# Performance work log

Hardware: AMD Instinct MI355X
Metric: run time of the kernel (lower is better)

Reference implementation:

```python
import jax, jax.numpy as jnp
import numpy as np

def setup_inputs() -> dict:
    key = jax.random.key(0)
    QKV = jax.random.normal(key, (3, 2, 8, 4096, 64), dtype=jnp.float32)
    return {"QKV": QKV}

def reference(QKV):
    Q, K, V = QKV[0], QKV[1], QKV[2]            # each [B, H, N, d]
    scores = jnp.einsum('bhnd,bhmd->bhnm', Q, K)  # full N x N score matrix (no scaling, matching source)
    attn = jax.nn.softmax(scores, axis=-1)
    return jnp.einsum('bhnm,bhmd->bhnd', attn, V)
```

## Files before the change

### kernel.cpp

```cpp
#include <hip/hip_runtime.h>


typedef _Float16 f16x8 __attribute__((ext_vector_type(8)));
typedef _Float16 f16x2 __attribute__((ext_vector_type(2)));
typedef short s16x8 __attribute__((ext_vector_type(8)));
typedef short s16x4 __attribute__((ext_vector_type(4)));
typedef float f32x4 __attribute__((ext_vector_type(4)));

#define NHEADS 16
#define SEQ 4096
#define HDIM 64
#define BR 256
#define NH 4
#define BC 64
#define KP 72
#define PP 72
#define NSPLIT 2
#define MPAD 4.0f

__device__ __forceinline__ float fast_exp2(float x) {
#if __has_builtin(__builtin_amdgcn_exp2f)
  return __builtin_amdgcn_exp2f(x);
#else
  return exp2f(x);
#endif
}

__device__ __forceinline__ f16x2 pkrtz(float a, float b) {
  return __builtin_bit_cast(f16x2, __builtin_amdgcn_cvt_pkrtz(a, b));
}

__device__ __forceinline__ unsigned short f2bf(float f) {
  unsigned u = __builtin_bit_cast(unsigned, f);
  u += 0x7fffu + ((u >> 16) & 1u);
  return (unsigned short)(u >> 16);
}

__device__ __forceinline__ unsigned bfpack2(float a, float b) {
  return (__builtin_bit_cast(unsigned, b) & 0xffff0000u) |
         (__builtin_bit_cast(unsigned, a) >> 16);
}

__global__ __launch_bounds__(256) void prep(const float* __restrict__ QKV,
                                            _Float16* __restrict__ K16,
                                            short* __restrict__ Vt) {
  const size_t tensElems = (size_t)NHEADS * SEQ * HDIM;
  __shared__ __align__(16) short T[64 * KP];
  if (blockIdx.x < 2048) {
    const float* Kf = QKV + tensElems;
    size_t i = ((size_t)blockIdx.x * 256 + threadIdx.x) * 8;
    float4 a = *(const float4*)(Kf + i);
    float4 b = *(const float4*)(Kf + i + 4);
    union { f16x8 v; f16x2 h2[4]; } u;
    u.h2[0] = pkrtz(a.x, a.y);
    u.h2[1] = pkrtz(a.z, a.w);
    u.h2[2] = pkrtz(b.x, b.y);
    u.h2[3] = pkrtz(b.z, b.w);
    *(f16x8*)(K16 + i) = u.v;
  } else {
    const int vb = blockIdx.x - 2048;
    const int bh = vb >> 6;
    const int nt = vb & 63;
    const float* Vh = QKV + 2 * tensElems + (size_t)bh * SEQ * HDIM +
                      (size_t)nt * 64 * HDIM;
    const int t = threadIdx.x;
    #pragma unroll
    for (int p = 0; p < 4; ++p) {
      int idx = t + p * 256;
      int row = idx >> 4, c4 = (idx & 15) << 2;
      float4 v = *(const float4*)(Vh + row * HDIM + c4);
      s16x4 h;
      h[0] = (short)f2bf(v.x); h[1] = (short)f2bf(v.y);
      h[2] = (short)f2bf(v.z); h[3] = (short)f2bf(v.w);
      *(s16x4*)&T[row * KP + c4] = h;
    }
    __syncthreads();
    const int d = t & 63, w = t >> 6;
    s16x8 o0, o1;
    #pragma unroll
    for (int j = 0; j < 8; ++j) o0[j] = T[(w * 16 + j) * KP + d];
    #pragma unroll
    for (int j = 0; j < 8; ++j) o1[j] = T[(w * 16 + 8 + j) * KP + d];
    short* out = Vt + (size_t)bh * HDIM * SEQ + (size_t)d * SEQ + nt * 64 + w * 16;
    *(s16x8*)out = o0;
    *(s16x8*)(out + 8) = o1;
  }
}

__global__ __launch_bounds__(256) void combine2(const _Float16* __restrict__ Op,
                                                const float2* __restrict__ Ml,
                                                float* __restrict__ O) {
  const size_t tensElems = (size_t)NHEADS * SEQ * HDIM;
  size_t t = (size_t)blockIdx.x * 256 + threadIdx.x;
  size_t row = t >> 3;
  int seg = (int)(t & 7) << 3;
  float2 s0 = Ml[row];
  float2 s1 = Ml[(size_t)NHEADS * SEQ + row];
  float Ms = fmaxf(s0.x, s1.x);
  float a0 = fast_exp2(s0.x - Ms) * s0.y;
  float a1 = fast_exp2(s1.x - Ms) * s1.y;
  float inv = 1.0f / (a0 + a1);
  a0 *= inv;
  a1 *= inv;
  f16x8 o0 = *(const f16x8*)(Op + row * HDIM + seg);
  f16x8 o1 = *(const f16x8*)(Op + tensElems + row * HDIM + seg);
  float4 r0, r1;
  r0.x = (float)o0[0] * a0 + (float)o1[0] * a1;
  r0.y = (float)o0[1] * a0 + (float)o1[1] * a1;
  r0.z = (float)o0[2] * a0 + (float)o1[2] * a1;
  r0.w = (float)o0[3] * a0 + (float)o1[3] * a1;
  r1.x = (float)o0[4] * a0 + (float)o1[4] * a1;
  r1.y = (float)o0[5] * a0 + (float)o1[5] * a1;
  r1.z = (float)o0[6] * a0 + (float)o1[6] * a1;
  r1.w = (float)o0[7] * a0 + (float)o1[7] * a1;
  *(float4*)(O + row * HDIM + seg) = r0;
  *(float4*)(O + row * HDIM + seg + 4) = r1;
}

template <bool PRE, bool SPLIT>
__global__ __launch_bounds__(256, 2) void flash_attn(const float* __restrict__ QKV,
                                                     const _Float16* __restrict__ K16g,
                                                     const short* __restrict__ Vt16,
                                                     float* __restrict__ Out,
                                                     _Float16* __restrict__ Opart,
                                                     float2* __restrict__ Ml) {
  const size_t headElems = (size_t)SEQ * HDIM;
  const size_t tensElems = (size_t)NHEADS * headElems;
  const int bh = blockIdx.x & 15;
  const int qt = blockIdx.x >> 4;
  const int split = SPLIT ? blockIdx.y : 0;
  const int ktBeg = SPLIT ? split * (SEQ / BC / NSPLIT) : 0;
  const int ktN = SPLIT ? (SEQ / BC / NSPLIT) : (SEQ / BC);

  const float* Q = QKV + (size_t)bh * headElems;
  const float* Kf = QKV + tensElems + (size_t)bh * headElems;
  const float* Vf = QKV + 2 * tensElems + (size_t)bh * headElems;
  const _Float16* Kg16 = K16g + (size_t)bh * headElems;
  const short* Vg16 = Vt16 + (size_t)bh * headElems;
  float* O = Out + (size_t)bh * headElems;

  const int tid = threadIdx.x;
  const int wave = tid >> 6;
  const int lane = tid & 63;
  const int g = lane >> 4;
  const int l16 = lane & 15;

  __shared__ __align__(16) _Float16 Ks[BC * KP];
  __shared__ __align__(16) short Vs[HDIM * KP];
  __shared__ __align__(16) short Ps[4][NH][16 * PP];

  const float LOG2E = 1.4426950408889634f;
  const int qbase = qt * BR + wave * (16 * NH);
  f16x8 qf[NH][2];
  #pragma unroll
  for (int h = 0; h < NH; ++h) {
    const float* qp = Q + (size_t)(qbase + h * 16 + l16) * HDIM + g * 8;
    #pragma unroll
    for (int c = 0; c < 2; ++c) {
      float4 a = *(const float4*)(qp + c * 32);
      float4 b = *(const float4*)(qp + c * 32 + 4);
      union { f16x8 v; f16x2 h2[4]; } u;
      u.h2[0] = pkrtz(a.x * LOG2E, a.y * LOG2E);
      u.h2[1] = pkrtz(a.z * LOG2E, a.w * LOG2E);
      u.h2[2] = pkrtz(b.x * LOG2E, b.y * LOG2E);
      u.h2[3] = pkrtz(b.z * LOG2E, b.w * LOG2E);
      qf[h][c] = u.v;
    }
  }

  const int sr = tid >> 2;
  const int sc = (tid & 3) << 4;

  s16x8 kpre[2];
  s16x8 vpre[2];

  auto prefetch = [&](int kt) {
    if constexpr (PRE) {
      const _Float16* kg = Kg16 + (size_t)(kt * BC + sr) * HDIM + sc;
      kpre[0] = *(const s16x8*)(kg);
      kpre[1] = *(const s16x8*)(kg + 8);
      const short* vg = Vg16 + (size_t)sr * SEQ + kt * BC + sc;
      vpre[0] = *(const s16x8*)(vg);
      vpre[1] = *(const s16x8*)(vg + 8);
    }
  };
  auto commit = [&](int kt) {
    if constexpr (PRE) {
      *(s16x8*)&Ks[sr * KP + sc] = kpre[0];
      *(s16x8*)&Ks[sr * KP + sc + 8] = kpre[1];
      *(s16x8*)&Vs[sr * KP + sc] = vpre[0];
      *(s16x8*)&Vs[sr * KP + sc + 8] = vpre[1];
    } else {
      const float* kg = Kf + (size_t)(kt * BC + sr) * HDIM + sc;
      float4 a = *(const float4*)(kg), b = *(const float4*)(kg + 4);
      float4 c = *(const float4*)(kg + 8), d = *(const float4*)(kg + 12);
      union { f16x8 v; f16x2 h2[4]; } ka, kb;
      ka.h2[0] = pkrtz(a.x, a.y);
      ka.h2[1] = pkrtz(a.z, a.w);
      ka.h2[2] = pkrtz(b.x, b.y);
      ka.h2[3] = pkrtz(b.z, b.w);
      kb.h2[0] = pkrtz(c.x, c.y);
      kb.h2[1] = pkrtz(c.z, c.w);
      kb.h2[2] = pkrtz(d.x, d.y);
      kb.h2[3] = pkrtz(d.z, d.w);
      *(f16x8*)&Ks[sr * KP + sc] = ka.v;
      *(f16x8*)&Ks[sr * KP + sc + 8] = kb.v;
      const float* vg = Vf + (size_t)(kt * BC + sr) * HDIM + sc;
      float4 va = *(const float4*)(vg), vb = *(const float4*)(vg + 4);
      float4 vc = *(const float4*)(vg + 8), vd = *(const float4*)(vg + 12);
      float vv[16] = {va.x, va.y, va.z, va.w, vb.x, vb.y, vb.z, vb.w,
                      vc.x, vc.y, vc.z, vc.w, vd.x, vd.y, vd.z, vd.w};
      #pragma unroll
      for (int j = 0; j < 16; ++j) Vs[(sc + j) * KP + sr] = (short)f2bf(vv[j]);
    }
  };

  f32x4 acc[NH][4];
  #pragma unroll
  for (int h = 0; h < NH; ++h)
    #pragma unroll
    for (int nt = 0; nt < 4; ++nt)
      #pragma unroll
      for (int i = 0; i < 4; ++i) acc[h][nt][i] = 0.f;
  float l_[NH] = {0.f, 0.f, 0.f, 0.f};
  float negM[NH] = {0.f, 0.f, 0.f, 0.f};

  prefetch(ktBeg);
  commit(ktBeg);

  for (int it = 0; it < ktN; ++it) {
    const int kt = ktBeg + it;
    __syncthreads();
    if (it < ktN - 1) prefetch(kt + 1);

    f32x4 s[NH][4];
    #pragma unroll
    for (int jt = 0; jt < 4; ++jt) {
      const int ka = (jt * 16 + l16) * KP + g * 8;
      f16x8 k0 = *(const f16x8*)&Ks[ka];
      f16x8 k1 = *(const f16x8*)&Ks[ka + 32];
      #pragma unroll
      for (int h = 0; h < NH; ++h) {
        f32x4 z;
        z[0] = z[1] = z[2] = z[3] = negM[h];
        z = __builtin_amdgcn_mfma_f32_16x16x32_f16(k0, qf[h][0], z, 0, 0, 0);
        z = __builtin_amdgcn_mfma_f32_16x16x32_f16(k1, qf[h][1], z, 0, 0, 0);
        s[h][jt] = z;
      }
    }

    if (it == 0) {
      #pragma unroll
      for (int h = 0; h < NH; ++h) {
        float mx = s[h][0][0];
        #pragma unroll
        for (int jt = 0; jt < 4; ++jt)
          #pragma unroll
          for (int ri = 0; ri < 4; ++ri) mx = fmaxf(mx, s[h][jt][ri]);
        mx = fmaxf(mx, __shfl_xor(mx, 16));
        mx = fmaxf(mx, __shfl_xor(mx, 32));
        negM[h] = -(mx + MPAD);
        #pragma unroll
        for (int jt = 0; jt < 4; ++jt)
          #pragma unroll
          for (int ri = 0; ri < 4; ++ri) s[h][jt][ri] += negM[h];
      }
    }

    #pragma unroll
    for (int h = 0; h < NH; ++h) {
      float psum = l_[h];
      const int e0 = l16 * PP + 4 * g;
      #pragma unroll
      for (int jt = 0; jt < 4; ++jt) {
        float p0 = fast_exp2(s[h][jt][0]);
        float p1 = fast_exp2(s[h][jt][1]);
        float p2 = fast_exp2(s[h][jt][2]);
        float p3 = fast_exp2(s[h][jt][3]);
        psum += (p0 + p1) + (p2 + p3);
        uint2 w;
        w.x = bfpack2(p0, p1);
        w.y = bfpack2(p2, p3);
        *(uint2*)&Ps[wave][h][e0 + jt * 16] = w;
      }
      l_[h] = psum;
    }

    s16x8 pa[NH][2];
    #pragma unroll
    for (int h = 0; h < NH; ++h) {
      pa[h][0] = *(const s16x8*)&Ps[wave][h][l16 * PP + g * 8];
      pa[h][1] = *(const s16x8*)&Ps[wave][h][l16 * PP + g * 8 + 32];
    }
    #pragma unroll
    for (int nt = 0; nt < 4; ++nt) {
      const int va = (nt * 16 + l16) * KP + g * 8;
      s16x8 v0 = *(const s16x8*)&Vs[va];
      s16x8 v1 = *(const s16x8*)&Vs[va + 32];
      #pragma unroll
      for (int h = 0; h < NH; ++h) {
        acc[h][nt] = __builtin_amdgcn_mfma_f32_16x16x32_bf16(pa[h][0], v0, acc[h][nt], 0, 0, 0);
        acc[h][nt] = __builtin_amdgcn_mfma_f32_16x16x32_bf16(pa[h][1], v1, acc[h][nt], 0, 0, 0);
      }
    }

    __syncthreads();
    if (it < ktN - 1) commit(kt + 1);
  }

  #pragma unroll
  for (int h = 0; h < NH; ++h) {
    float lf = l_[h];
    lf += __shfl_xor(lf, 16);
    lf += __shfl_xor(lf, 32);
    float linv = 1.0f / lf;
    if constexpr (SPLIT) {
      if (g == 0) {
        Ml[(size_t)split * NHEADS * SEQ + (size_t)bh * SEQ + qbase + h * 16 + l16] =
            float2{-negM[h], lf};
      }
      _Float16* op = Opart + (size_t)split * tensElems + (size_t)bh * headElems;
      #pragma unroll
      for (int ri = 0; ri < 4; ++ri) {
        float lB = __shfl(linv, 4 * g + ri);
        const int row = qbase + h * 16 + 4 * g + ri;
        #pragma unroll
        for (int nt = 0; nt < 4; ++nt)
          op[(size_t)row * HDIM + nt * 16 + l16] = (_Float16)(acc[h][nt][ri] * lB);
      }
    } else {
      #pragma unroll
      for (int ri = 0; ri < 4; ++ri) {
        float lB = __shfl(linv, 4 * g + ri);
        const int row = qbase + h * 16 + 4 * g + ri;
        #pragma unroll
        for (int nt = 0; nt < 4; ++nt)
          O[(size_t)row * HDIM + nt * 16 + l16] = acc[h][nt][ri] * lB;
      }
    }
  }
}

extern "C" void kernel_launch(void* const* d_in, const int* in_sizes, int n_in,
                              void* d_out, int out_size, void* d_ws, size_t ws_size,
                              hipStream_t stream) {
  const float* QKV = (const float*)d_in[0];
  float* Out = (float*)d_out;
  const size_t tensElems = (size_t)NHEADS * SEQ * HDIM;
  const size_t k16Bytes = tensElems * sizeof(_Float16);
  const size_t vtBytes = tensElems * sizeof(short);
  const size_t opBytes = (size_t)NSPLIT * tensElems * sizeof(_Float16);
  const size_t mlBytes = (size_t)NSPLIT * NHEADS * SEQ * 8;

  dim3 block(256);

  if (ws_size >= k16Bytes + vtBytes + opBytes + mlBytes) {
    _Float16* K16 = (_Float16*)d_ws;
    short* Vt16 = (short*)((char*)d_ws + k16Bytes);
    _Float16* Opart = (_Float16*)((char*)d_ws + k16Bytes + vtBytes);
    float2* Ml = (float2*)((char*)d_ws + k16Bytes + vtBytes + opBytes);
    hipLaunchKernelGGL(prep, dim3(3072), block, 0, stream, QKV, K16, Vt16);
    hipLaunchKernelGGL((flash_attn<true, true>), dim3(NHEADS * (SEQ / BR), NSPLIT),
                       block, 0, stream, QKV, K16, Vt16, Out, Opart, Ml);
    hipLaunchKernelGGL(combine2, dim3((NHEADS * SEQ * HDIM / 8) / 256), block, 0,
                       stream, Opart, Ml, Out);
  } else {
    hipLaunchKernelGGL((flash_attn<false, false>), dim3(NHEADS * (SEQ / BR)), block,
                       0, stream, QKV, (const _Float16*)nullptr,
                       (const short*)nullptr, Out, (_Float16*)nullptr,
                       (float2*)nullptr);
  }
}
```

Measured before the change: 170.7 us.

## Drop KV split-combine; use 128-row query tiles with 2-wave blocks

Removes the two-way KV split and the separate combine kernel. Parallelism now comes from halving the query tile to 128 rows with 128-thread blocks, giving 512 blocks that each sweep the full key sequence. This eliminates the fp16 partial-output round trip through global memory and one kernel launch. In exchange, each K/V tile staged in LDS is shared by only two waves instead of four, so K/V load traffic per query row doubles. The V-transpose write pattern in prep is also reorganised so each thread writes contiguous 16-element segments.

```diff
diff --git a/kernel.cpp b/kernel.cpp
--- a/kernel.cpp
+++ b/kernel.cpp
@@ -10,12 +10,11 @@
 #define NHEADS 16
 #define SEQ 4096
 #define HDIM 64
-#define BR 256
+#define BR 128
 #define NH 4
 #define BC 64
 #define KP 72
 #define PP 72
-#define NSPLIT 2
 #define MPAD 4.0f
 
 __device__ __forceinline__ float fast_exp2(float x) {
@@ -75,62 +74,27 @@
       *(s16x4*)&T[row * KP + c4] = h;
     }
     __syncthreads();
-    const int d = t & 63, w = t >> 6;
+    const int d = t >> 2, nc = (t & 3) << 4;
     s16x8 o0, o1;
     #pragma unroll
-    for (int j = 0; j < 8; ++j) o0[j] = T[(w * 16 + j) * KP + d];
-    #pragma unroll
-    for (int j = 0; j < 8; ++j) o1[j] = T[(w * 16 + 8 + j) * KP + d];
-    short* out = Vt + (size_t)bh * HDIM * SEQ + (size_t)d * SEQ + nt * 64 + w * 16;
+    for (int j = 0; j < 8; ++j) o0[j] = T[(nc + j) * KP + d];
+    #pragma unroll
+    for (int j = 0; j < 8; ++j) o1[j] = T[(nc + 8 + j) * KP + d];
+    short* out = Vt + (size_t)bh * HDIM * SEQ + (size_t)d * SEQ + nt * 64 + nc;
     *(s16x8*)out = o0;
     *(s16x8*)(out + 8) = o1;
   }
 }
 
-__global__ __launch_bounds__(256) void combine2(const _Float16* __restrict__ Op,
-                                                const float2* __restrict__ Ml,
-                                                float* __restrict__ O) {
-  const size_t tensElems = (size_t)NHEADS * SEQ * HDIM;
-  size_t t = (size_t)blockIdx.x * 256 + threadIdx.x;
-  size_t row = t >> 3;
-  int seg = (int)(t & 7) << 3;
-  float2 s0 = Ml[row];
-  float2 s1 = Ml[(size_t)NHEADS * SEQ + row];
-  float Ms = fmaxf(s0.x, s1.x);
-  float a0 = fast_exp2(s0.x - Ms) * s0.y;
-  float a1 = fast_exp2(s1.x - Ms) * s1.y;
-  float inv = 1.0f / (a0 + a1);
-  a0 *= inv;
-  a1 *= inv;
-  f16x8 o0 = *(const f16x8*)(Op + row * HDIM + seg);
-  f16x8 o1 = *(const f16x8*)(Op + tensElems + row * HDIM + seg);
-  float4 r0, r1;
-  r0.x = (float)o0[0] * a0 + (float)o1[0] * a1;
-  r0.y = (float)o0[1] * a0 + (float)o1[1] * a1;
-  r0.z = (float)o0[2] * a0 + (float)o1[2] * a1;
-  r0.w = (float)o0[3] * a0 + (float)o1[3] * a1;
-  r1.x = (float)o0[4] * a0 + (float)o1[4] * a1;
-  r1.y = (float)o0[5] * a0 + (float)o1[5] * a1;
-  r1.z = (float)o0[6] * a0 + (float)o1[6] * a1;
-  r1.w = (float)o0[7] * a0 + (float)o1[7] * a1;
-  *(float4*)(O + row * HDIM + seg) = r0;
-  *(float4*)(O + row * HDIM + seg + 4) = r1;
-}
-
-template <bool PRE, bool SPLIT>
-__global__ __launch_bounds__(256, 2) void flash_attn(const float* __restrict__ QKV,
+template <bool PRE>
+__global__ __launch_bounds__(128, 2) void flash_attn(const float* __restrict__ QKV,
                                                      const _Float16* __restrict__ K16g,
                                                      const short* __restrict__ Vt16,
-                                                     float* __restrict__ Out,
-                                                     _Float16* __restrict__ Opart,
-                                                     float2* __restrict__ Ml) {
+                                                     float* __restrict__ Out) {
   const size_t headElems = (size_t)SEQ * HDIM;
   const size_t tensElems = (size_t)NHEADS * headElems;
   const int bh = blockIdx.x & 15;
   const int qt = blockIdx.x >> 4;
-  const int split = SPLIT ? blockIdx.y : 0;
-  const int ktBeg = SPLIT ? split * (SEQ / BC / NSPLIT) : 0;
-  const int ktN = SPLIT ? (SEQ / BC / NSPLIT) : (SEQ / BC);
 
   const float* Q = QKV + (size_t)bh * headElems;
   const float* Kf = QKV + tensElems + (size_t)bh * headElems;
@@ -147,7 +111,7 @@
 
   __shared__ __align__(16) _Float16 Ks[BC * KP];
   __shared__ __align__(16) short Vs[HDIM * KP];
-  __shared__ __align__(16) short Ps[4][NH][16 * PP];
+  __shared__ __align__(16) short Ps[2][NH][16 * PP];
 
   const float LOG2E = 1.4426950408889634f;
   const int qbase = qt * BR + wave * (16 * NH);
@@ -168,50 +132,58 @@
     }
   }
 
-  const int sr = tid >> 2;
-  const int sc = (tid & 3) << 4;
-
-  s16x8 kpre[2];
-  s16x8 vpre[2];
+  const int sr = tid >> 1;
+  const int sc = (tid & 1) << 5;
+
+  s16x8 kpre[4];
+  s16x8 vpre[4];
 
   auto prefetch = [&](int kt) {
     if constexpr (PRE) {
       const _Float16* kg = Kg16 + (size_t)(kt * BC + sr) * HDIM + sc;
       kpre[0] = *(const s16x8*)(kg);
       kpre[1] = *(const s16x8*)(kg + 8);
+      kpre[2] = *(const s16x8*)(kg + 16);
+      kpre[3] = *(const s16x8*)(kg + 24);
       const short* vg = Vg16 + (size_t)sr * SEQ + kt * BC + sc;
       vpre[0] = *(const s16x8*)(vg);
       vpre[1] = *(const s16x8*)(vg + 8);
+      vpre[2] = *(const s16x8*)(vg + 16);
+      vpre[3] = *(const s16x8*)(vg + 24);
     }
   };
   auto commit = [&](int kt) {
     if constexpr (PRE) {
       *(s16x8*)&Ks[sr * KP + sc] = kpre[0];
       *(s16x8*)&Ks[sr * KP + sc + 8] = kpre[1];
+      *(s16x8*)&Ks[sr * KP + sc + 16] = kpre[2];
+      *(s16x8*)&Ks[sr * KP + sc + 24] = kpre[3];
       *(s16x8*)&Vs[sr * KP + sc] = vpre[0];
       *(s16x8*)&Vs[sr * KP + sc + 8] = vpre[1];
+      *(s16x8*)&Vs[sr * KP + sc + 16] = vpre[2];
+      *(s16x8*)&Vs[sr * KP + sc + 24] = vpre[3];
     } else {
       const float* kg = Kf + (size_t)(kt * BC + sr) * HDIM + sc;
-      float4 a = *(const float4*)(kg), b = *(const float4*)(kg + 4);
-      float4 c = *(const float4*)(kg + 8), d = *(const float4*)(kg + 12);
-      union { f16x8 v; f16x2 h2[4]; } ka, kb;
-      ka.h2[0] = pkrtz(a.x, a.y);
-      ka.h2[1] = pkrtz(a.z, a.w);
-      ka.h2[2] = pkrtz(b.x, b.y);
-      ka.h2[3] = pkrtz(b.z, b.w);
-      kb.h2[0] = pkrtz(c.x, c.y);
-      kb.h2[1] = pkrtz(c.z, c.w);
-      kb.h2[2] = pkrtz(d.x, d.y);
-      kb.h2[3] = pkrtz(d.z, d.w);
-      *(f16x8*)&Ks[sr * KP + sc] = ka.v;
-      *(f16x8*)&Ks[sr * KP + sc + 8] = kb.v;
+      #pragma unroll
+      for (int q4 = 0; q4 < 4; ++q4) {
+        float4 a = *(const float4*)(kg + q4 * 8);
+        float4 b = *(const float4*)(kg + q4 * 8 + 4);
+        union { f16x8 v; f16x2 h2[4]; } ka;
+        ka.h2[0] = pkrtz(a.x, a.y);
+        ka.h2[1] = pkrtz(a.z, a.w);
+        ka.h2[2] = pkrtz(b.x, b.y);
+        ka.h2[3] = pkrtz(b.z, b.w);
+        *(f16x8*)&Ks[sr * KP + sc + q4 * 8] = ka.v;
+      }
       const float* vg = Vf + (size_t)(kt * BC + sr) * HDIM + sc;
-      float4 va = *(const float4*)(vg), vb = *(const float4*)(vg + 4);
-      float4 vc = *(const float4*)(vg + 8), vd = *(const float4*)(vg + 12);
-      float vv[16] = {va.x, va.y, va.z, va.w, vb.x, vb.y, vb.z, vb.w,
-                      vc.x, vc.y, vc.z, vc.w, vd.x, vd.y, vd.z, vd.w};
-      #pragma unroll
-      for (int j = 0; j < 16; ++j) Vs[(sc + j) * KP + sr] = (short)f2bf(vv[j]);
+      #pragma unroll
+      for (int q4 = 0; q4 < 8; ++q4) {
+        float4 v = *(const float4*)(vg + q4 * 4);
+        Vs[(sc + q4 * 4 + 0) * KP + sr] = (short)f2bf(v.x);
+        Vs[(sc + q4 * 4 + 1) * KP + sr] = (short)f2bf(v.y);
+        Vs[(sc + q4 * 4 + 2) * KP + sr] = (short)f2bf(v.z);
+        Vs[(sc + q4 * 4 + 3) * KP + sr] = (short)f2bf(v.w);
+      }
     }
   };
 
@@ -225,13 +197,12 @@
   float l_[NH] = {0.f, 0.f, 0.f, 0.f};
   float negM[NH] = {0.f, 0.f, 0.f, 0.f};
 
-  prefetch(ktBeg);
-  commit(ktBeg);
-
-  for (int it = 0; it < ktN; ++it) {
-    const int kt = ktBeg + it;
+  prefetch(0);
+  commit(0);
+
+  for (int it = 0; it < SEQ / BC; ++it) {
     __syncthreads();
-    if (it < ktN - 1) prefetch(kt + 1);
+    if (it < SEQ / BC - 1) prefetch(it + 1);
 
     f32x4 s[NH][4];
     #pragma unroll
@@ -305,7 +276,7 @@
     }
 
     __syncthreads();
-    if (it < ktN - 1) commit(kt + 1);
+    if (it < SEQ / BC - 1) commit(it + 1);
   }
 
   #pragma unroll
@@ -314,29 +285,13 @@
     lf += __shfl_xor(lf, 16);
     lf += __shfl_xor(lf, 32);
     float linv = 1.0f / lf;
-    if constexpr (SPLIT) {
-      if (g == 0) {
-        Ml[(size_t)split * NHEADS * SEQ + (size_t)bh * SEQ + qbase + h * 16 + l16] =
-            float2{-negM[h], lf};
-      }
-      _Float16* op = Opart + (size_t)split * tensElems + (size_t)bh * headElems;
-      #pragma unroll
-      for (int ri = 0; ri < 4; ++ri) {
-        float lB = __shfl(linv, 4 * g + ri);
-        const int row = qbase + h * 16 + 4 * g + ri;
-        #pragma unroll
-        for (int nt = 0; nt < 4; ++nt)
-          op[(size_t)row * HDIM + nt * 16 + l16] = (_Float16)(acc[h][nt][ri] * lB);
-      }
-    } else {
-      #pragma unroll
-      for (int ri = 0; ri < 4; ++ri) {
-        float lB = __shfl(linv, 4 * g + ri);
-        const int row = qbase + h * 16 + 4 * g + ri;
-        #pragma unroll
-        for (int nt = 0; nt < 4; ++nt)
-          O[(size_t)row * HDIM + nt * 16 + l16] = acc[h][nt][ri] * lB;
-      }
+    #pragma unroll
+    for (int ri = 0; ri < 4; ++ri) {
+      float lB = __shfl(linv, 4 * g + ri);
+      const int row = qbase + h * 16 + 4 * g + ri;
+      #pragma unroll
+      for (int nt = 0; nt < 4; ++nt)
+        O[(size_t)row * HDIM + nt * 16 + l16] = acc[h][nt][ri] * lB;
     }
   }
 }
@@ -349,25 +304,17 @@
   const size_t tensElems = (size_t)NHEADS * SEQ * HDIM;
   const size_t k16Bytes = tensElems * sizeof(_Float16);
   const size_t vtBytes = tensElems * sizeof(short);
-  const size_t opBytes = (size_t)NSPLIT * tensElems * sizeof(_Float16);
-  const size_t mlBytes = (size_t)NSPLIT * NHEADS * SEQ * 8;
-
-  dim3 block(256);
-
-  if (ws_size >= k16Bytes + vtBytes + opBytes + mlBytes) {
+
+  dim3 grid(NHEADS * (SEQ / BR));
+
+  if (ws_size >= k16Bytes + vtBytes) {
     _Float16* K16 = (_Float16*)d_ws;
     short* Vt16 = (short*)((char*)d_ws + k16Bytes);
-    _Float16* Opart = (_Float16*)((char*)d_ws + k16Bytes + vtBytes);
-    float2* Ml = (float2*)((char*)d_ws + k16Bytes + vtBytes + opBytes);
-    hipLaunchKernelGGL(prep, dim3(3072), block, 0, stream, QKV, K16, Vt16);
-    hipLaunchKernelGGL((flash_attn<true, true>), dim3(NHEADS * (SEQ / BR), NSPLIT),
-                       block, 0, stream, QKV, K16, Vt16, Out, Opart, Ml);
-    hipLaunchKernelGGL(combine2, dim3((NHEADS * SEQ * HDIM / 8) / 256), block, 0,
-                       stream, Opart, Ml, Out);
+    hipLaunchKernelGGL(prep, dim3(3072), dim3(256), 0, stream, QKV, K16, Vt16);
+    hipLaunchKernelGGL((flash_attn<true>), grid, dim3(128), 0, stream, QKV, K16,
+                       Vt16, Out);
   } else {
-    hipLaunchKernelGGL((flash_attn<false, false>), dim3(NHEADS * (SEQ / BR)), block,
-                       0, stream, QKV, (const _Float16*)nullptr,
-                       (const short*)nullptr, Out, (_Float16*)nullptr,
-                       (float2*)nullptr);
-  }
-}
+    hipLaunchKernelGGL((flash_attn<false>), grid, dim3(128), 0, stream, QKV,
+                       (const _Float16*)nullptr, (const short*)nullptr, Out);
+  }
+}
```

After: 220.8 us. 29.3% more time.
